# Kernel tuning notes

Measured on AMD Instinct MI355X. Metric: run time of the kernel, lower is better.

## Reference

```python
import jax, jax.numpy as jnp
import numpy as np

NUM_HEADS = 8
SIZES = [(80, 80), (40, 40), (20, 20), (10, 10), (5, 5)]


def _ln(x, g, b):
    m = x.mean(-1, keepdims=True)
    var = ((x - m) ** 2).mean(-1, keepdims=True)
    return (x - m) / jnp.sqrt(var + 1e-5) * g + b


def setup_inputs() -> dict:
    key = jax.random.key(0)
    ks = jax.random.split(key, 24)
    bs, c, S = 2, 256, 1024  # v_dim = embed_dim = c
    d = {}
    for i, (h, w) in enumerate(SIZES):
        d[f"q{i}"] = jax.random.normal(ks[i], (bs, c, h, w), jnp.float32)
    d["cache"] = jax.random.normal(ks[5], (bs, S, c), jnp.float32)
    d["mask"] = jax.random.randint(ks[6], (bs, S), 0, 2).astype(jnp.int32)
    d["ln_v_g"] = jnp.ones((c,), jnp.float32)
    d["ln_v_b"] = jnp.zeros((c,), jnp.float32)
    d["ln_c_g"] = jnp.ones((c,), jnp.float32)
    d["ln_c_b"] = jnp.zeros((c,), jnp.float32)
    sd = c ** -0.5
    d["Wv"] = jax.random.normal(ks[7], (c, c), jnp.float32) * sd
    d["bv"] = jnp.zeros((c,), jnp.float32)
    d["Wc"] = jax.random.normal(ks[8], (c, c), jnp.float32) * sd
    d["bc"] = jnp.zeros((c,), jnp.float32)
    d["Wvc"] = jax.random.normal(ks[9], (c, c), jnp.float32) * sd
    d["bvc"] = jnp.zeros((c,), jnp.float32)
    d["Wo"] = jax.random.normal(ks[10], (c, c), jnp.float32) * sd
    d["bo"] = jnp.zeros((c,), jnp.float32)
    d["Wg1"] = jax.random.normal(ks[11], (c, c // 2), jnp.float32) * sd
    d["bg1"] = jnp.zeros((c // 2,), jnp.float32)
    d["Wg2"] = jax.random.normal(ks[12], (c // 2, c), jnp.float32) * 0.01
    d["bg2"] = jnp.zeros((c,), jnp.float32)
    return d


def _forward(q0, q1, q2, q3, q4, cache, mask, ln_v_g, ln_v_b, ln_c_g, ln_c_b,
             Wv, bv, Wc, bc, Wvc, bvc, Wo, bo, Wg1, bg1, Wg2, bg2):
    feats = [q0, q1, q2, q3, q4]
    bs = q0.shape[0]
    sizes = [(f.shape[2], f.shape[3]) for f in feats]
    # permute_and_flatten: (bs, c, h, w) -> (bs, h*w, c), concat over levels
    v = jnp.concatenate(
        [f.reshape(bs, f.shape[1], -1).transpose(0, 2, 1) for f in feats], axis=1)
    T = v.shape[1]
    E = Wv.shape[1]
    hd = E // NUM_HEADS
    scale = hd ** -0.5

    vn = _ln(v, ln_v_g, ln_v_b)
    cn = _ln(cache, ln_c_g, ln_c_b)

    q = ((vn @ Wv + bv) * scale).reshape(bs, T, NUM_HEADS, hd).transpose(0, 2, 1, 3)
    k = (cn @ Wc + bc).reshape(bs, -1, NUM_HEADS, hd).transpose(0, 2, 1, 3)
    val = (cn @ Wvc + bvc).reshape(bs, -1, NUM_HEADS, hd).transpose(0, 2, 1, 3)

    attn = jnp.einsum('bhtd,bhsd->bhts', q, k)
    attn = jnp.clip(attn, -50000.0, 50000.0)
    mf = mask.astype(attn.dtype)  # (bs, S); zeros -> -9e15, ones kept as +1.0 (faithful)
    attn = attn + jnp.where(mf == 0, jnp.asarray(-9e15, attn.dtype), mf)[:, None, None, :]
    p = jax.nn.softmax(attn, axis=-1)  # dropout inactive in eval mode

    o = jnp.einsum('bhts,bhsd->bhtd', p, val).transpose(0, 2, 1, 3).reshape(bs, T, E)
    delta = o @ Wo + bo

    gate = jnp.tanh(jax.nn.relu(v @ Wg1 + bg1) @ Wg2 + bg2)
    new_v = (v + gate * delta).transpose(0, 2, 1)  # (bs, c, T)

    outs = []
    start = 0
    for h, w in sizes:
        outs.append(new_v[:, :, start:start + h * w].reshape(bs, -1, h, w))
        start += h * w
    return tuple(outs)


def reference(q0, q1, q2, q3, q4, cache, mask, ln_v_g, ln_v_b, ln_c_g, ln_c_b,
              Wv, bv, Wc, bc, Wvc, bvc, Wo, bo, Wg1, bg1, Wg2, bg2):
    return _forward(q0, q1, q2, q3, q4, cache, mask, ln_v_g, ln_v_b, ln_c_g, ln_c_b,
                    Wv, bv, Wc, bc, Wvc, bvc, Wo, bo, Wg1, bg1, Wg2, bg2)
```

## Files before the change

kernel.cpp:

```cpp
#include <hip/hip_runtime.h>
#include <hip/hip_bf16.h>
#include <math.h>


typedef __attribute__((ext_vector_type(8))) short short8;
typedef __attribute__((ext_vector_type(4))) float f32x4;
typedef __hip_bfloat16 bf16;

#define T_TOK 8525
#define S_TOK 1024
#define CDIM  256
#define NHEAD 8
#define BSZ   2

static __device__ __forceinline__ f32x4 mfma16(short8 a, short8 b, f32x4 c) {
  return __builtin_amdgcn_mfma_f32_16x16x32_bf16(a, b, c, 0, 0, 0);
}

static __device__ __forceinline__ float fexp2(float x) {
#if __has_builtin(__builtin_amdgcn_exp2f)
  return __builtin_amdgcn_exp2f(x);
#else
  return exp2f(x);
#endif
}

static __device__ __forceinline__ unsigned int pack_bf16(float a, float b) {
#if __has_builtin(__builtin_amdgcn_perm)
  return __builtin_amdgcn_perm(__float_as_uint(b), __float_as_uint(a), 0x07060302u);
#else
  return (__float_as_uint(a) >> 16) | (__float_as_uint(b) & 0xFFFF0000u);
#endif
}

__global__ __launch_bounds__(256) void stage1(
    const float* __restrict__ q0, const float* __restrict__ q1,
    const float* __restrict__ q2, const float* __restrict__ q3,
    const float* __restrict__ q4,
    const float* __restrict__ Wv, const float* __restrict__ Wc,
    const float* __restrict__ Wvc, const float* __restrict__ Wo,
    const float* __restrict__ Wg1, const float* __restrict__ Wg2,
    const float* __restrict__ bv, const float* __restrict__ bg1,
    const float* __restrict__ bc, const float* __restrict__ bvc,
    const float* __restrict__ cache, const int* __restrict__ mask,
    const float* __restrict__ ln_c_g, const float* __restrict__ ln_c_b,
    const float* __restrict__ ln_v_g, const float* __restrict__ ln_v_b,
    bf16* __restrict__ WqgT, bf16* __restrict__ WcvcT, bf16* __restrict__ WoT,
    bf16* __restrict__ Wg2T, float* __restrict__ biasCV,
    float* __restrict__ biasQG, unsigned int* __restrict__ mpk,
    bf16* __restrict__ cnb, bf16* __restrict__ vTb,
    bf16* __restrict__ vb, bf16* __restrict__ vnb) {
  __shared__ float sm[4160];
  const int bid = blockIdx.x, tid = threadIdx.x;
  if (bid == 80) {
    biasCV[tid] = bc[tid];
    biasCV[tid + 256] = bvc[tid];
    biasQG[tid] = bv[tid];
    if (tid < 128) biasQG[256 + tid] = bg1[tid];
#pragma unroll
    for (int j = tid; j < 1024; j += 256) {
      int bb = j >> 9, s2 = (j & 511) * 2;
      mpk[j] = (mask[bb * 1024 + s2] ? 0xFFFFu : 0u) |
               (mask[bb * 1024 + s2 + 1] ? 0xFFFF0000u : 0u);
    }
    return;
  }
  if (bid > 80 && bid < 593) {
    int lane = tid & 63;
    int row = (bid - 81) * 4 + (tid >> 6);
    const float* x = cache + (size_t)row * CDIM;
    float v0 = x[lane], v1 = x[lane + 64], v2 = x[lane + 128], v3 = x[lane + 192];
    float s = v0 + v1 + v2 + v3;
    float s2 = v0 * v0 + v1 * v1 + v2 * v2 + v3 * v3;
#pragma unroll
    for (int off = 1; off < 64; off <<= 1) {
      s += __shfl_xor(s, off);
      s2 += __shfl_xor(s2, off);
    }
    float mean = s * (1.f / 256.f);
    float var = s2 * (1.f / 256.f) - mean * mean;
    float rstd = rsqrtf(var + 1e-5f);
    bf16* y = cnb + (size_t)row * CDIM;
    y[lane] = __float2bfloat16((v0 - mean) * rstd * ln_c_g[lane] + ln_c_b[lane]);
    y[lane + 64] = __float2bfloat16((v1 - mean) * rstd * ln_c_g[lane + 64] + ln_c_b[lane + 64]);
    y[lane + 128] = __float2bfloat16((v2 - mean) * rstd * ln_c_g[lane + 128] + ln_c_b[lane + 128]);
    y[lane + 192] = __float2bfloat16((v3 - mean) * rstd * ln_c_g[lane + 192] + ln_c_b[lane + 192]);
    return;
  }
  if (bid < 80) {
    float (*tl)[65] = (float(*)[65])sm;
    const float* W; bf16* WT; int K, N, local;
    if (bid < 16)      { W = Wv;  WT = WqgT;           K = 256; N = 256; local = bid; }
    else if (bid < 32) { W = Wc;  WT = WcvcT;          K = 256; N = 256; local = bid - 16; }
    else if (bid < 48) { W = Wvc; WT = WcvcT + 65536;  K = 256; N = 256; local = bid - 32; }
    else if (bid < 64) { W = Wo;  WT = WoT;            K = 256; N = 256; local = bid - 48; }
    else if (bid < 72) { W = Wg1; WT = WqgT + 65536;   K = 256; N = 128; local = bid - 64; }
    else               { W = Wg2; WT = Wg2T;           K = 128; N = 256; local = bid - 72; }
    const int ktiles = K >> 6;
    const int K0 = (local % ktiles) * 64, N0 = (local / ktiles) * 64;
    const int kk = tid >> 4, n4 = (tid & 15) * 4;
#pragma unroll
    for (int i = 0; i < 4; ++i) {
      int k = kk + 16 * i;
      float4 w4 = *(const float4*)&W[(size_t)(K0 + k) * N + N0 + n4];
      tl[n4 + 0][k] = w4.x; tl[n4 + 1][k] = w4.y;
      tl[n4 + 2][k] = w4.z; tl[n4 + 3][k] = w4.w;
    }
    __syncthreads();
    const int nn = tid >> 4, k4 = (tid & 15) * 4;
#pragma unroll
    for (int i = 0; i < 4; ++i) {
      int n = nn + 16 * i;
      bf16 o[4] __attribute__((aligned(8)));
#pragma unroll
      for (int j = 0; j < 4; ++j) o[j] = __float2bfloat16(tl[n][k4 + j]);
      *(uint2*)&WT[(size_t)(N0 + n) * K + K0 + k4] = *(uint2*)o;
    }
    return;
  }
  constexpr int HW[5] = {6400, 1600, 400, 100, 25};
  constexpr int TST[5] = {0, 6400, 8000, 8400, 8500};
  constexpr int T16[5] = {0, 400, 500, 525, 532};
  float (*tile)[260] = (float(*)[260])sm;
  const int bb = bid - 593;
  const int tileid = bb % 534, b = bb / 534;
  int lvl = 0;
#pragma unroll
  for (int i = 1; i < 5; ++i) if (tileid >= T16[i]) lvl = i;
  const int p0 = (tileid - T16[lvl]) * 16;
  const int hw = HW[lvl];
  const float* src = ((lvl == 0) ? q0 : (lvl == 1) ? q1 : (lvl == 2) ? q2
                      : (lvl == 3) ? q3 : q4) + (size_t)b * CDIM * hw;
  const int pl = tid & 15, cb = tid >> 4;
  const int pg = p0 + pl;
#pragma unroll
  for (int i = 0; i < 16; ++i) {
    int c = cb + 16 * i;
    tile[pl][c] = (pg < hw) ? src[(size_t)c * hw + pg] : 0.f;
  }
  __syncthreads();
  if (pg < hw) {
    int tglob = TST[lvl] + pg;
#pragma unroll
    for (int i = 0; i < 16; ++i) {
      int c = cb + 16 * i;
      vTb[((size_t)b * CDIM + c) * T_TOK + tglob] = __float2bfloat16(tile[pl][c]);
    }
  }
  const int lane = tid & 63, w = tid >> 6;
#pragma unroll
  for (int rr = 0; rr < 4; ++rr) {
    int row = w * 4 + rr;
    int p = p0 + row;
    if (p >= hw) continue;
    float x0 = tile[row][lane], x1 = tile[row][lane + 64],
          x2 = tile[row][lane + 128], x3 = tile[row][lane + 192];
    float s = x0 + x1 + x2 + x3;
    float s2 = x0 * x0 + x1 * x1 + x2 * x2 + x3 * x3;
#pragma unroll
    for (int off = 1; off < 64; off <<= 1) {
      s += __shfl_xor(s, off);
      s2 += __shfl_xor(s2, off);
    }
    float mean = s * (1.f / 256.f);
    float var = s2 * (1.f / 256.f) - mean * mean;
    float rstd = rsqrtf(var + 1e-5f);
    size_t base = ((size_t)b * T_TOK + TST[lvl] + p) * CDIM;
    float xs[4] = {x0, x1, x2, x3};
#pragma unroll
    for (int j = 0; j < 4; ++j) {
      int c = lane + 64 * j;
      float x = xs[j];
      vb[base + c] = __float2bfloat16(x);
      vnb[base + c] = __float2bfloat16((x - mean) * rstd * ln_v_g[c] + ln_v_b[c]);
    }
  }
}

__global__ __launch_bounds__(256) void gemm_fused(
    const bf16* __restrict__ vnb, const bf16* __restrict__ vb,
    const bf16* __restrict__ WqgT, const float* __restrict__ biasQG,
    bf16* __restrict__ qb, bf16* __restrict__ ghb,
    const bf16* __restrict__ cnb, const bf16* __restrict__ WcvcT,
    const float* __restrict__ biasCV, bf16* __restrict__ kb,
    bf16* __restrict__ valTb) {
  __shared__ __align__(16) bf16 Asl[128][136];
  __shared__ __align__(16) bf16 Bsl[64][136];
  const int tid = threadIdx.x;
  const int wave = tid >> 6, lane = tid & 63, quad = lane >> 4, l15 = lane & 15;
  const int bid = blockIdx.x;
  const bool kval = bid >= 804;
  int m0, n0, M;
  const bf16 *A, *BW;
  const float* bias;
  if (!kval) {
    m0 = (bid / 6) * 128; n0 = (bid % 6) * 64;
    A = (n0 < 256) ? vnb : vb; BW = WqgT; bias = biasQG; M = BSZ * T_TOK;
  } else {
    int i = bid - 804;
    m0 = (i / 8) * 128; n0 = (i % 8) * 64;
    A = cnb; BW = WcvcT; bias = biasCV; M = BSZ * S_TOK;
  }
  f32x4 acc[2][4];
#pragma unroll
  for (int i = 0; i < 2; ++i)
#pragma unroll
    for (int j = 0; j < 4; ++j) acc[i][j] = (f32x4){0.f, 0.f, 0.f, 0.f};

  for (int k0 = 0; k0 < 256; k0 += 128) {
    __syncthreads();
#pragma unroll
    for (int c = 0; c < 8; ++c) {
      int chunk = c * 256 + tid;
      int row = chunk >> 4, col = (chunk & 15) * 8;
      int gr = m0 + row;
      if (gr >= M) gr = M - 1;
      *(uint4*)&Asl[row][col] = *(const uint4*)&A[(size_t)gr * 256 + k0 + col];
    }
#pragma unroll
    for (int c = 0; c < 4; ++c) {
      int chunk = c * 256 + tid;
      int row = chunk >> 4, col = (chunk & 15) * 8;
      *(uint4*)&Bsl[row][col] = *(const uint4*)&BW[(size_t)(n0 + row) * 256 + k0 + col];
    }
    __syncthreads();
#pragma unroll
    for (int kk = 0; kk < 128; kk += 32) {
      short8 af0 = *(const short8*)&Asl[wave * 32 + l15][kk + quad * 8];
      short8 af1 = *(const short8*)&Asl[wave * 32 + 16 + l15][kk + quad * 8];
      short8 bf0 = *(const short8*)&Bsl[l15][kk + quad * 8];
      short8 bf1 = *(const short8*)&Bsl[16 + l15][kk + quad * 8];
      short8 bf2 = *(const short8*)&Bsl[32 + l15][kk + quad * 8];
      short8 bf3 = *(const short8*)&Bsl[48 + l15][kk + quad * 8];
      acc[0][0] = mfma16(af0, bf0, acc[0][0]);
      acc[0][1] = mfma16(af0, bf1, acc[0][1]);
      acc[0][2] = mfma16(af0, bf2, acc[0][2]);
      acc[0][3] = mfma16(af0, bf3, acc[0][3]);
      acc[1][0] = mfma16(af1, bf0, acc[1][0]);
      acc[1][1] = mfma16(af1, bf1, acc[1][1]);
      acc[1][2] = mfma16(af1, bf2, acc[1][2]);
      acc[1][3] = mfma16(af1, bf3, acc[1][3]);
    }
  }
#pragma unroll
  for (int ms = 0; ms < 2; ++ms)
#pragma unroll
    for (int nt = 0; nt < 4; ++nt)
#pragma unroll
      for (int r = 0; r < 4; ++r) {
        int m = m0 + wave * 32 + ms * 16 + quad * 4 + r;
        if (m >= M) continue;
        int n = n0 + nt * 16 + l15;
        float x = acc[ms][nt][r] + bias[n];
        if (!kval) {
          if (n < 256) {
            qb[(size_t)m * 256 + n] = __float2bfloat16(x * 0.25504765517f);
          } else {
            ghb[(size_t)m * 128 + (n - 256)] = __float2bfloat16(fmaxf(x, 0.f));
          }
        } else {
          if (n < 256) {
            kb[(size_t)m * 256 + n] = __float2bfloat16(x);
          } else {
            int n2 = n - 256;
            int bb = m >> 10, s = m & 1023;
            int hh = n2 >> 5, d = n2 & 31;
            valTb[(((size_t)(bb * NHEAD + hh) * 32 + d) << 10) + s] = __float2bfloat16(x);
          }
        }
      }
}

__global__ __launch_bounds__(512) void attn_kernel(
    const bf16* __restrict__ qb, const bf16* __restrict__ kb,
    const bf16* __restrict__ valTb, const unsigned int* __restrict__ mpk,
    bf16* __restrict__ ob) {
  __shared__ __align__(16) bf16 Ksl[2][4096];
  __shared__ __align__(16) bf16 Vsl[2][4096];
  const int tid = threadIdx.x;
  const int lane = tid & 63, wv = tid >> 6, quad = lane >> 4, l15 = lane & 15;
  const int b = blockIdx.y >> 3, h = blockIdx.y & 7;
  const int t0w = blockIdx.x * 128 + wv * 16;
  int tA = t0w + l15;
  if (tA >= T_TOK) tA = T_TOK - 1;
  short8 qf = *(const short8*)&qb[((size_t)b * T_TOK + tA) * CDIM + h * 32 + quad * 8];
  f32x4 o0 = {0.f, 0.f, 0.f, 0.f};
  f32x4 o1 = {0.f, 0.f, 0.f, 0.f};
  f32x4 o2 = {0.f, 0.f, 0.f, 0.f};
  const f32x4 zero4 = {0.f, 0.f, 0.f, 0.f};
  const short8 ones = (short8){0x3F80, 0x3F80, 0x3F80, 0x3F80,
                               0x3F80, 0x3F80, 0x3F80, 0x3F80};
  const size_t kbase = ((size_t)b * S_TOK) * CDIM + h * 32;
  const size_t vbase = (size_t)(b * NHEAD + h) << 15;
  const unsigned int* mrow = mpk + b * 512;
  const int ks = tid >> 2, kd16 = tid & 3;
  const int kdst = (ks >> 4) * 512 + (ks & 15) * 32 + kd16 * 8;
  const size_t kofs = (size_t)ks * CDIM + kd16 * 8;
  const int vd = tid >> 4, vs8 = (tid & 15) * 8;
  const int schunk = vs8 >> 5, sb_ = vs8 & 31;
  const int kb1 = (((sb_ >> 2) & 3) << 3) + (((sb_ >> 4) & 1) << 2);
  const int sb2_ = sb_ + 4;
  const int kb2 = (((sb2_ >> 2) & 3) << 3) + (((sb2_ >> 4) & 1) << 2);
  const int vbl = schunk * 1024 + (vd >> 4) * 512 + (vd & 15) * 32;
  const int vd1 = vbl + kb1, vd2 = vbl + kb2;
  const size_t vofs = ((size_t)vd << 10) + vs8;

  uint4 kreg = *(const uint4*)&kb[kbase + kofs];
  uint4 vreg = *(const uint4*)&valTb[vbase + vofs];
  *(uint4*)&Ksl[0][kdst] = kreg;
  {
    uint2 lo; lo.x = vreg.x; lo.y = vreg.y;
    uint2 hi; hi.x = vreg.z; hi.y = vreg.w;
    *(uint2*)&Vsl[0][vd1] = lo;
    *(uint2*)&Vsl[0][vd2] = hi;
  }
  __syncthreads();

  for (int sbi = 0; sbi < 8; ++sbi) {
    const int cur = sbi & 1;
    if (sbi < 7) {
      int sb = (sbi + 1) * 128;
      kreg = *(const uint4*)&kb[kbase + (size_t)sb * CDIM + kofs];
      vreg = *(const uint4*)&valTb[vbase + sb + vofs];
    }
    const unsigned int* mchunk = mrow + sbi * 64;
#pragma unroll
    for (int ss = 0; ss < 128; ss += 32) {
      const int cb = (ss >> 5) * 1024 + l15 * 32 + quad * 8;
      short8 kf0 = *(const short8*)&Ksl[cur][cb];
      short8 kf1 = *(const short8*)&Ksl[cur][cb + 512];
      short8 vf0 = *(const short8*)&Vsl[cur][cb];
      short8 vf1 = *(const short8*)&Vsl[cur][cb + 512];
      uint2 mk0 = *(const uint2*)&mchunk[(ss >> 1) + quad * 2];
      uint2 mk1 = *(const uint2*)&mchunk[(ss >> 1) + 8 + quad * 2];
      f32x4 s0 = mfma16(kf0, qf, zero4);
      f32x4 s1 = mfma16(kf1, qf, zero4);
      float pa = fexp2(s0[0]), pb = fexp2(s0[1]);
      float pc = fexp2(s0[2]), pd = fexp2(s0[3]);
      float pe = fexp2(s1[0]), pf_ = fexp2(s1[1]);
      float pg = fexp2(s1[2]), ph = fexp2(s1[3]);
      uint4 pu;
      pu.x = pack_bf16(pa, pb) & mk0.x;
      pu.y = pack_bf16(pc, pd) & mk0.y;
      pu.z = pack_bf16(pe, pf_) & mk1.x;
      pu.w = pack_bf16(pg, ph) & mk1.y;
      short8 pfr = *(short8*)&pu;
      o2 = mfma16(pfr, ones, o2);
      o0 = mfma16(pfr, vf0, o0);
      o1 = mfma16(pfr, vf1, o1);
    }
    if (sbi < 7) {
      const int nxt = cur ^ 1;
      *(uint4*)&Ksl[nxt][kdst] = kreg;
      uint2 lo; lo.x = vreg.x; lo.y = vreg.y;
      uint2 hi; hi.x = vreg.z; hi.y = vreg.w;
      *(uint2*)&Vsl[nxt][vd1] = lo;
      *(uint2*)&Vsl[nxt][vd2] = hi;
    }
    __syncthreads();
  }
  bf16* tile = &Ksl[0][0] + wv * 512;
#pragma unroll
  for (int r = 0; r < 4; ++r) {
    float rli = 1.0f / o2[r];
    int tl = quad * 4 + r;
    tile[tl * 32 + l15] = __float2bfloat16(o0[r] * rli);
    tile[tl * 32 + 16 + l15] = __float2bfloat16(o1[r] * rli);
  }
  {
    int tl = lane >> 2;
    int d8 = (lane & 3) * 8;
    int t = t0w + tl;
    uint4 val = *(const uint4*)&tile[tl * 32 + d8];
    if (t < T_TOK)
      *(uint4*)&ob[((size_t)b * T_TOK + t) * CDIM + h * 32 + d8] = val;
  }
}

__global__ __launch_bounds__(256) void gemm_out(
    const bf16* __restrict__ obuf, const bf16* __restrict__ WoT,
    const float* __restrict__ bo, const bf16* __restrict__ ghb,
    const bf16* __restrict__ Wg2T, const float* __restrict__ bg2,
    const bf16* __restrict__ vTb, float* __restrict__ out, int M) {
  constexpr int HW[5] = {6400, 1600, 400, 100, 25};
  constexpr int TST[5] = {0, 6400, 8000, 8400, 8500};
  constexpr size_t OUTOFF[5] = {0, 3276800, 4096000, 4300800, 4352000};
  __shared__ __align__(16) char smem[52224];
  bf16 (*Asl)[136] = (bf16(*)[136])smem;
  bf16 (*Bsl)[136] = (bf16(*)[136])(smem + 34816);
  float (*tile)[132] = (float(*)[132])smem;
  const int tid = threadIdx.x;
  const int wave = tid >> 6, lane = tid & 63, quad = lane >> 4, l15 = lane & 15;
  const int m0 = blockIdx.y * 128, n0 = blockIdx.x * 64;
  f32x4 aD[2][4], aG[2][4];
#pragma unroll
  for (int i = 0; i < 2; ++i)
#pragma unroll
    for (int j = 0; j < 4; ++j) {
      aD[i][j] = (f32x4){0.f, 0.f, 0.f, 0.f};
      aG[i][j] = (f32x4){0.f, 0.f, 0.f, 0.f};
    }
  for (int k0 = 0; k0 < 256; k0 += 128) {
    __syncthreads();
#pragma unroll
    for (int c = 0; c < 8; ++c) {
      int chunk = c * 256 + tid;
      int row = chunk >> 4, col = (chunk & 15) * 8;
      int gr = m0 + row;
      if (gr >= M) gr = M - 1;
      *(uint4*)&Asl[row][col] = *(const uint4*)&obuf[(size_t)gr * 256 + k0 + col];
    }
#pragma unroll
    for (int c = 0; c < 4; ++c) {
      int chunk = c * 256 + tid;
      int row = chunk >> 4, col = (chunk & 15) * 8;
      *(uint4*)&Bsl[row][col] = *(const uint4*)&WoT[(size_t)(n0 + row) * 256 + k0 + col];
    }
    __syncthreads();
#pragma unroll
    for (int kk = 0; kk < 128; kk += 32) {
      short8 af0 = *(const short8*)&Asl[wave * 32 + l15][kk + quad * 8];
      short8 af1 = *(const short8*)&Asl[wave * 32 + 16 + l15][kk + quad * 8];
#pragma unroll
      for (int j = 0; j < 4; ++j) {
        short8 bfj = *(const short8*)&Bsl[j * 16 + l15][kk + quad * 8];
        aD[0][j] = mfma16(af0, bfj, aD[0][j]);
        aD[1][j] = mfma16(af1, bfj, aD[1][j]);
      }
    }
  }
  __syncthreads();
#pragma unroll
  for (int c = 0; c < 8; ++c) {
    int chunk = c * 256 + tid;
    int row = chunk >> 4, col = (chunk & 15) * 8;
    int gr = m0 + row;
    if (gr >= M) gr = M - 1;
    *(uint4*)&Asl[row][col] = *(const uint4*)&ghb[(size_t)gr * 128 + col];
  }
#pragma unroll
  for (int c = 0; c < 4; ++c) {
    int chunk = c * 256 + tid;
    int row = chunk >> 4, col = (chunk & 15) * 8;
    *(uint4*)&Bsl[row][col] = *(const uint4*)&Wg2T[(size_t)(n0 + row) * 128 + col];
  }
  __syncthreads();
#pragma unroll
  for (int kk = 0; kk < 128; kk += 32) {
    short8 af0 = *(const short8*)&Asl[wave * 32 + l15][kk + quad * 8];
    short8 af1 = *(const short8*)&Asl[wave * 32 + 16 + l15][kk + quad * 8];
#pragma unroll
    for (int j = 0; j < 4; ++j) {
      short8 bfj = *(const short8*)&Bsl[j * 16 + l15][kk + quad * 8];
      aG[0][j] = mfma16(af0, bfj, aG[0][j]);
      aG[1][j] = mfma16(af1, bfj, aG[1][j]);
    }
  }
  __syncthreads();
#pragma unroll
  for (int ms = 0; ms < 2; ++ms)
#pragma unroll
    for (int nt = 0; nt < 4; ++nt) {
      int n = n0 + nt * 16 + l15;
      float bod = bo[n], bgd = bg2[n];
      float4 res;
      float tmp[4];
#pragma unroll
      for (int r = 0; r < 4; ++r) {
        float xd = aD[ms][nt][r] + bod;
        float xg = aG[ms][nt][r] + bgd;
        float xc = fminf(fmaxf(xg, -15.f), 15.f);
        float e = __expf(2.f * xc);
        float gt = (e - 1.f) / (e + 1.f);
        tmp[r] = gt * xd;
      }
      res.x = tmp[0]; res.y = tmp[1]; res.z = tmp[2]; res.w = tmp[3];
      *(float4*)&tile[nt * 16 + l15][wave * 32 + ms * 16 + quad * 4] = res;
    }
  __syncthreads();
  const int tl = tid & 127, c2 = tid >> 7;
  const int t = m0 + tl;
  const bool valid = t < M;
  int bb = (t >= T_TOK) ? 1 : 0;
  int tt = t - bb * T_TOK;
  if (tt >= T_TOK) tt = T_TOK - 1;
  int lvl = 0;
#pragma unroll
  for (int i = 1; i < 5; ++i) if (tt >= TST[i]) lvl = i;
  const int p = tt - TST[lvl], hw = HW[lvl];
  float* dst = out + OUTOFF[lvl] + ((size_t)bb * CDIM + n0) * hw + p;
  const bf16* vsrc = vTb + ((size_t)bb * CDIM + n0) * T_TOK + tt;
#pragma unroll
  for (int c0 = 0; c0 < 32; ++c0) {
    int c = c0 * 2 + c2;
    if (valid)
      dst[(size_t)c * hw] = __bfloat162float(vsrc[(size_t)c * T_TOK]) + tile[c][tl];
  }
}

extern "C" void kernel_launch(void* const* d_in, const int* in_sizes, int n_in,
                              void* d_out, int out_size, void* d_ws, size_t ws_size,
                              hipStream_t stream) {
  const float* q0 = (const float*)d_in[0];
  const float* q1 = (const float*)d_in[1];
  const float* q2 = (const float*)d_in[2];
  const float* q3 = (const float*)d_in[3];
  const float* q4 = (const float*)d_in[4];
  const float* cache = (const float*)d_in[5];
  const int* mask = (const int*)d_in[6];
  const float* ln_v_g = (const float*)d_in[7];
  const float* ln_v_b = (const float*)d_in[8];
  const float* ln_c_g = (const float*)d_in[9];
  const float* ln_c_b = (const float*)d_in[10];
  const float* Wv = (const float*)d_in[11];
  const float* bv = (const float*)d_in[12];
  const float* Wc = (const float*)d_in[13];
  const float* bc = (const float*)d_in[14];
  const float* Wvc = (const float*)d_in[15];
  const float* bvc = (const float*)d_in[16];
  const float* Wo = (const float*)d_in[17];
  const float* bo = (const float*)d_in[18];
  const float* Wg1 = (const float*)d_in[19];
  const float* bg1 = (const float*)d_in[20];
  const float* Wg2 = (const float*)d_in[21];
  const float* bg2 = (const float*)d_in[22];
  float* out = (float*)d_out;

  const int R = BSZ * T_TOK;
  const size_t RC = (size_t)R * CDIM;
  const size_t SC = (size_t)BSZ * S_TOK * CDIM;

  char* p = (char*)d_ws;
  bf16* vTb = (bf16*)p;            p += RC * 2;
  bf16* vb = (bf16*)p;             p += RC * 2;
  bf16* vnb = (bf16*)p;            p += RC * 2;
  bf16* qb = (bf16*)p;             p += RC * 2;
  bf16* ob = (bf16*)p;             p += RC * 2;
  bf16* ghb = (bf16*)p;            p += (size_t)R * 128 * 2;
  bf16* cnb = (bf16*)p;            p += SC * 2;
  bf16* kb = (bf16*)p;             p += SC * 2;
  bf16* valTb = (bf16*)p;          p += SC * 2;
  bf16* WqgT = (bf16*)p;           p += 98304 * 2;
  bf16* WcvcT = (bf16*)p;          p += 131072 * 2;
  bf16* WoT = (bf16*)p;            p += 65536 * 2;
  bf16* Wg2T = (bf16*)p;           p += 32768 * 2;
  float* biasCV = (float*)p;       p += 512 * 4;
  float* biasQG = (float*)p;       p += 384 * 4;
  unsigned int* mpk = (unsigned int*)p; p += 1024 * 4;

  stage1<<<dim3(1661), dim3(256), 0, stream>>>(
      q0, q1, q2, q3, q4, Wv, Wc, Wvc, Wo, Wg1, Wg2, bv, bg1, bc, bvc,
      cache, mask, ln_c_g, ln_c_b, ln_v_g, ln_v_b,
      WqgT, WcvcT, WoT, Wg2T, biasCV, biasQG, mpk, cnb, vTb, vb, vnb);
  gemm_fused<<<dim3(932), dim3(256), 0, stream>>>(
      vnb, vb, WqgT, biasQG, qb, ghb, cnb, WcvcT, biasCV, kb, valTb);
  attn_kernel<<<dim3(67, BSZ * NHEAD), dim3(512), 0, stream>>>(
      qb, kb, valTb, mpk, ob);
  gemm_out<<<dim3(4, 134), dim3(256), 0, stream>>>(
      ob, WoT, bo, ghb, Wg2T, bg2, vTb, out, R);
}
```

Measured before the change: 205.9 us.

## Fold LayerNorm into projection GEMMs via per-row stats and weight scaling

```diff
diff --git a/kernel.cpp b/kernel.cpp
--- a/kernel.cpp
+++ b/kernel.cpp
@@ -40,29 +40,46 @@
     const float* __restrict__ Wv, const float* __restrict__ Wc,
     const float* __restrict__ Wvc, const float* __restrict__ Wo,
     const float* __restrict__ Wg1, const float* __restrict__ Wg2,
-    const float* __restrict__ bv, const float* __restrict__ bg1,
-    const float* __restrict__ bc, const float* __restrict__ bvc,
+    const float* __restrict__ bv, const float* __restrict__ bc,
+    const float* __restrict__ bvc,
     const float* __restrict__ cache, const int* __restrict__ mask,
     const float* __restrict__ ln_c_g, const float* __restrict__ ln_c_b,
     const float* __restrict__ ln_v_g, const float* __restrict__ ln_v_b,
     bf16* __restrict__ WqgT, bf16* __restrict__ WcvcT, bf16* __restrict__ WoT,
-    bf16* __restrict__ Wg2T, float* __restrict__ biasCV,
-    float* __restrict__ biasQG, unsigned int* __restrict__ mpk,
-    bf16* __restrict__ cnb, bf16* __restrict__ vTb,
-    bf16* __restrict__ vb, bf16* __restrict__ vnb) {
+    bf16* __restrict__ Wg2T, float2* __restrict__ foldQ,
+    float2* __restrict__ foldCV, unsigned int* __restrict__ mpk,
+    bf16* __restrict__ cacheb, float2* __restrict__ rowstatC,
+    bf16* __restrict__ vTb, bf16* __restrict__ vb,
+    float2* __restrict__ rowstatV) {
   __shared__ float sm[4160];
   const int bid = blockIdx.x, tid = threadIdx.x;
   if (bid == 80) {
-    biasCV[tid] = bc[tid];
-    biasCV[tid + 256] = bvc[tid];
-    biasQG[tid] = bv[tid];
-    if (tid < 128) biasQG[256 + tid] = bg1[tid];
+    float cs = 0.f, bt = 0.f;
+    for (int k = 0; k < 256; ++k) {
+      float w = Wv[k * 256 + tid];
+      cs += ln_v_g[k] * w;
+      bt += ln_v_b[k] * w;
+    }
+    foldQ[tid] = make_float2(cs, bt + bv[tid]);
 #pragma unroll
     for (int j = tid; j < 1024; j += 256) {
       int bb = j >> 9, s2 = (j & 511) * 2;
       mpk[j] = (mask[bb * 1024 + s2] ? 0xFFFFu : 0u) |
                (mask[bb * 1024 + s2 + 1] ? 0xFFFF0000u : 0u);
     }
+    return;
+  }
+  if (bid >= 1661) {
+    const float* W = (bid == 1661) ? Wc : Wvc;
+    const float* bb_ = (bid == 1661) ? bc : bvc;
+    int base = (bid == 1661) ? 0 : 256;
+    float cs = 0.f, bt = 0.f;
+    for (int k = 0; k < 256; ++k) {
+      float w = W[k * 256 + tid];
+      cs += ln_c_g[k] * w;
+      bt += ln_c_b[k] * w;
+    }
+    foldCV[base + tid] = make_float2(cs, bt + bb_[tid]);
     return;
   }
   if (bid > 80 && bid < 593) {
@@ -80,19 +97,21 @@
     float mean = s * (1.f / 256.f);
     float var = s2 * (1.f / 256.f) - mean * mean;
     float rstd = rsqrtf(var + 1e-5f);
-    bf16* y = cnb + (size_t)row * CDIM;
-    y[lane] = __float2bfloat16((v0 - mean) * rstd * ln_c_g[lane] + ln_c_b[lane]);
-    y[lane + 64] = __float2bfloat16((v1 - mean) * rstd * ln_c_g[lane + 64] + ln_c_b[lane + 64]);
-    y[lane + 128] = __float2bfloat16((v2 - mean) * rstd * ln_c_g[lane + 128] + ln_c_b[lane + 128]);
-    y[lane + 192] = __float2bfloat16((v3 - mean) * rstd * ln_c_g[lane + 192] + ln_c_b[lane + 192]);
+    bf16* y = cacheb + (size_t)row * CDIM;
+    y[lane] = __float2bfloat16(v0);
+    y[lane + 64] = __float2bfloat16(v1);
+    y[lane + 128] = __float2bfloat16(v2);
+    y[lane + 192] = __float2bfloat16(v3);
+    if (lane == 0) rowstatC[row] = make_float2(rstd, rstd * mean);
     return;
   }
   if (bid < 80) {
     float (*tl)[65] = (float(*)[65])sm;
     const float* W; bf16* WT; int K, N, local;
-    if (bid < 16)      { W = Wv;  WT = WqgT;           K = 256; N = 256; local = bid; }
-    else if (bid < 32) { W = Wc;  WT = WcvcT;          K = 256; N = 256; local = bid - 16; }
-    else if (bid < 48) { W = Wvc; WT = WcvcT + 65536;  K = 256; N = 256; local = bid - 32; }
+    const float* gs = nullptr;
+    if (bid < 16)      { W = Wv;  WT = WqgT;           K = 256; N = 256; local = bid;       gs = ln_v_g; }
+    else if (bid < 32) { W = Wc;  WT = WcvcT;          K = 256; N = 256; local = bid - 16;  gs = ln_c_g; }
+    else if (bid < 48) { W = Wvc; WT = WcvcT + 65536;  K = 256; N = 256; local = bid - 32;  gs = ln_c_g; }
     else if (bid < 64) { W = Wo;  WT = WoT;            K = 256; N = 256; local = bid - 48; }
     else if (bid < 72) { W = Wg1; WT = WqgT + 65536;   K = 256; N = 128; local = bid - 64; }
     else               { W = Wg2; WT = Wg2T;           K = 128; N = 256; local = bid - 72; }
@@ -102,9 +121,10 @@
 #pragma unroll
     for (int i = 0; i < 4; ++i) {
       int k = kk + 16 * i;
+      float gk = gs ? gs[K0 + k] : 1.0f;
       float4 w4 = *(const float4*)&W[(size_t)(K0 + k) * N + N0 + n4];
-      tl[n4 + 0][k] = w4.x; tl[n4 + 1][k] = w4.y;
-      tl[n4 + 2][k] = w4.z; tl[n4 + 3][k] = w4.w;
+      tl[n4 + 0][k] = w4.x * gk; tl[n4 + 1][k] = w4.y * gk;
+      tl[n4 + 2][k] = w4.z * gk; tl[n4 + 3][k] = w4.w * gk;
     }
     __syncthreads();
     const int nn = tid >> 4, k4 = (tid & 15) * 4;
@@ -165,25 +185,26 @@
     float mean = s * (1.f / 256.f);
     float var = s2 * (1.f / 256.f) - mean * mean;
     float rstd = rsqrtf(var + 1e-5f);
-    size_t base = ((size_t)b * T_TOK + TST[lvl] + p) * CDIM;
+    size_t rowg = (size_t)b * T_TOK + TST[lvl] + p;
+    size_t base = rowg * CDIM;
     float xs[4] = {x0, x1, x2, x3};
 #pragma unroll
     for (int j = 0; j < 4; ++j) {
       int c = lane + 64 * j;
-      float x = xs[j];
-      vb[base + c] = __float2bfloat16(x);
-      vnb[base + c] = __float2bfloat16((x - mean) * rstd * ln_v_g[c] + ln_v_b[c]);
-    }
+      vb[base + c] = __float2bfloat16(xs[j]);
+    }
+    if (lane == 0) rowstatV[rowg] = make_float2(rstd, rstd * mean);
   }
 }
 
 __global__ __launch_bounds__(256) void gemm_fused(
-    const bf16* __restrict__ vnb, const bf16* __restrict__ vb,
-    const bf16* __restrict__ WqgT, const float* __restrict__ biasQG,
-    bf16* __restrict__ qb, bf16* __restrict__ ghb,
-    const bf16* __restrict__ cnb, const bf16* __restrict__ WcvcT,
-    const float* __restrict__ biasCV, bf16* __restrict__ kb,
-    bf16* __restrict__ valTb) {
+    const bf16* __restrict__ vb, const bf16* __restrict__ WqgT,
+    const float2* __restrict__ foldQ, const float2* __restrict__ rowstatV,
+    const float* __restrict__ bg1, bf16* __restrict__ qb,
+    bf16* __restrict__ ghb,
+    const bf16* __restrict__ cacheb, const bf16* __restrict__ WcvcT,
+    const float2* __restrict__ foldCV, const float2* __restrict__ rowstatC,
+    bf16* __restrict__ kb, bf16* __restrict__ valTb) {
   __shared__ __align__(16) bf16 Asl[128][136];
   __shared__ __align__(16) bf16 Bsl[64][136];
   const int tid = threadIdx.x;
@@ -192,14 +213,13 @@
   const bool kval = bid >= 804;
   int m0, n0, M;
   const bf16 *A, *BW;
-  const float* bias;
   if (!kval) {
     m0 = (bid / 6) * 128; n0 = (bid % 6) * 64;
-    A = (n0 < 256) ? vnb : vb; BW = WqgT; bias = biasQG; M = BSZ * T_TOK;
+    A = vb; BW = WqgT; M = BSZ * T_TOK;
   } else {
     int i = bid - 804;
     m0 = (i / 8) * 128; n0 = (i % 8) * 64;
-    A = cnb; BW = WcvcT; bias = biasCV; M = BSZ * S_TOK;
+    A = cacheb; BW = WcvcT; M = BSZ * S_TOK;
   }
   f32x4 acc[2][4];
 #pragma unroll
@@ -251,14 +271,21 @@
         int m = m0 + wave * 32 + ms * 16 + quad * 4 + r;
         if (m >= M) continue;
         int n = n0 + nt * 16 + l15;
-        float x = acc[ms][nt][r] + bias[n];
+        float a = acc[ms][nt][r];
         if (!kval) {
           if (n < 256) {
+            float2 f = foldQ[n];
+            float2 rs = rowstatV[m];
+            float x = rs.x * a - rs.y * f.x + f.y;
             qb[(size_t)m * 256 + n] = __float2bfloat16(x * 0.25504765517f);
           } else {
+            float x = a + bg1[n - 256];
             ghb[(size_t)m * 128 + (n - 256)] = __float2bfloat16(fmaxf(x, 0.f));
           }
         } else {
+          float2 f = foldCV[n];
+          float2 rs = rowstatC[m];
+          float x = rs.x * a - rs.y * f.x + f.y;
           if (n < 256) {
             kb[(size_t)m * 256 + n] = __float2bfloat16(x);
           } else {
@@ -533,27 +560,30 @@
   char* p = (char*)d_ws;
   bf16* vTb = (bf16*)p;            p += RC * 2;
   bf16* vb = (bf16*)p;             p += RC * 2;
-  bf16* vnb = (bf16*)p;            p += RC * 2;
   bf16* qb = (bf16*)p;             p += RC * 2;
   bf16* ob = (bf16*)p;             p += RC * 2;
   bf16* ghb = (bf16*)p;            p += (size_t)R * 128 * 2;
-  bf16* cnb = (bf16*)p;            p += SC * 2;
+  bf16* cacheb = (bf16*)p;         p += SC * 2;
   bf16* kb = (bf16*)p;             p += SC * 2;
   bf16* valTb = (bf16*)p;          p += SC * 2;
   bf16* WqgT = (bf16*)p;           p += 98304 * 2;
   bf16* WcvcT = (bf16*)p;          p += 131072 * 2;
   bf16* WoT = (bf16*)p;            p += 65536 * 2;
   bf16* Wg2T = (bf16*)p;           p += 32768 * 2;
-  float* biasCV = (float*)p;       p += 512 * 4;
-  float* biasQG = (float*)p;       p += 384 * 4;
+  float2* foldQ = (float2*)p;      p += 256 * 8;
+  float2* foldCV = (float2*)p;     p += 512 * 8;
+  float2* rowstatV = (float2*)p;   p += (size_t)R * 8;
+  float2* rowstatC = (float2*)p;   p += 2048 * 8;
   unsigned int* mpk = (unsigned int*)p; p += 1024 * 4;
 
-  stage1<<<dim3(1661), dim3(256), 0, stream>>>(
-      q0, q1, q2, q3, q4, Wv, Wc, Wvc, Wo, Wg1, Wg2, bv, bg1, bc, bvc,
+  stage1<<<dim3(1663), dim3(256), 0, stream>>>(
+      q0, q1, q2, q3, q4, Wv, Wc, Wvc, Wo, Wg1, Wg2, bv, bc, bvc,
       cache, mask, ln_c_g, ln_c_b, ln_v_g, ln_v_b,
-      WqgT, WcvcT, WoT, Wg2T, biasCV, biasQG, mpk, cnb, vTb, vb, vnb);
+      WqgT, WcvcT, WoT, Wg2T, foldQ, foldCV, mpk, cacheb, rowstatC,
+      vTb, vb, rowstatV);
   gemm_fused<<<dim3(932), dim3(256), 0, stream>>>(
-      vnb, vb, WqgT, biasQG, qb, ghb, cnb, WcvcT, biasCV, kb, valTb);
+      vb, WqgT, foldQ, rowstatV, bg1, qb, ghb,
+      cacheb, WcvcT, foldCV, rowstatC, kb, valTb);
   attn_kernel<<<dim3(67, BSZ * NHEAD), dim3(512), 0, stream>>>(
       qb, kb, valTb, mpk, ob);
   gemm_out<<<dim3(4, 134), dim3(256), 0, stream>>>(
```

Result: slower. 212.3 us (+3.1%).
